# Optimization experiments

Measured on AMD Instinct MI355X. Metric: run time of the kernel, lower is better.

The kernel has to match this reference:

```python
import jax, jax.numpy as jnp
import numpy as np

# ---- static configuration (mirrors init_kwargs) ----
B, V, C, NH, HD = 1, 6, 256, 8, 32     # batch, views, embed, heads, head_dim
Z, L, P = 4, 4, 2                       # z-ref points, fmap levels, ref points
BEV_H, BEV_W = 80, 80
Q = BEV_H * BEV_W
IMG_H, IMG_W = 480, 800
LEVEL_SHAPES = [(60, 100), (30, 50), (15, 25), (8, 13)]
S = sum(h * w for h, w in LEVEL_SHAPES)
RES = 0.512
OFFSET_SCALE = 1.0
FF = 512


def layer_norm(x, g, b):
    m = jnp.mean(x, -1, keepdims=True)
    v = jnp.var(x, -1, keepdims=True)
    return (x - m) / jnp.sqrt(v + 1e-5) * g + b


def _bev_grid():
    xs = (jnp.arange(BEV_W) + 0.5) / BEV_W
    ys = (jnp.arange(BEV_H) + 0.5) / BEV_H
    gy, gx = jnp.meshgrid(ys, xs, indexing='ij')
    ref = jnp.stack([gx.reshape(-1), gy.reshape(-1)], -1)        # (Q,2) normalized xy
    world = (ref - 0.5) * jnp.array([BEV_W * RES, BEV_H * RES])  # (Q,2) ego-frame meters
    return ref, world


def deform_sample(value, H, W, loc):
    """Bilinear sampling. value: (N, H*W, NH, HD); loc: (N, Qn, NH, PP, 2) in [0,1].
    Returns (N, Qn, NH, PP, HD); out-of-bounds samples contribute zero."""
    v = jnp.moveaxis(value, 2, 1)                                # (N, NH, HW, HD)
    x = loc[..., 0] * W - 0.5
    y = loc[..., 1] * H - 0.5
    x0 = jnp.floor(x); y0 = jnp.floor(y)
    lx, ly = x - x0, y - y0
    x0 = x0.astype(jnp.int32); y0 = y0.astype(jnp.int32)
    gather = jax.vmap(jax.vmap(lambda vt, it: vt[it]))           # over (N, NH)
    def corner(xi, yi, w):
        ok = ((xi >= 0) & (xi < W) & (yi >= 0) & (yi < H)).astype(value.dtype)
        idx = jnp.clip(yi, 0, H - 1) * W + jnp.clip(xi, 0, W - 1)
        g = gather(v, jnp.moveaxis(idx, 2, 1))                   # (N,NH,Qn,PP,HD)
        return jnp.moveaxis(g, 1, 2) * (w * ok)[..., None]
    return (corner(x0, y0, (1 - lx) * (1 - ly)) + corner(x0 + 1, y0, lx * (1 - ly))
            + corner(x0, y0 + 1, (1 - lx) * ly) + corner(x0 + 1, y0 + 1, lx * ly))


def _forward(bev_queries, bev_histories, multiscale_fmaps, transition_matrices, z_refs,
             cam_proj_matrices, Wv_t, Woff_t, boff_t, Ww_t, bw_t, Wo_t, bo_t, ln1_g, ln1_b,
             Wv_s, Woff_s, boff_s, Ww_s, bw_s, Wo_s, bo_s, ln2_g, ln2_b,
             W1, b1, W2, b2, ln3_g, ln3_b):
    ref, world = _bev_grid()
    q = bev_queries
    # ---------- temporal self-attention (deformable over current + warped history) ----------
    vcur = (q @ Wv_t).reshape(B, Q, NH, HD)
    vhist = (bev_histories @ Wv_t).reshape(B, Q, NH, HD)
    off_t = (q @ Woff_t + boff_t).reshape(B, Q, NH, 2, P, 2) * OFFSET_SCALE
    w_t = jax.nn.softmax((q @ Ww_t + bw_t).reshape(B, Q, NH, 2 * P), -1).reshape(B, Q, NH, 2, P)
    ext = jnp.array([BEV_W * RES, BEV_H * RES], jnp.float32)
    wh = jnp.concatenate([world, jnp.ones((Q, 1), jnp.float32)], -1)     # (Q,3)
    warped = jnp.einsum('bij,qj->bqi', transition_matrices, wh)          # (B,Q,3)
    ref_hist = warped[..., :2] / warped[..., 2:3] / ext + 0.5            # (B,Q,2)
    norm_bev = jnp.array([BEV_W, BEV_H], jnp.float32)
    loc_c = ref[None, :, None, None, :] + off_t[:, :, :, 0] / norm_bev
    loc_h = ref_hist[:, :, None, None, :] + off_t[:, :, :, 1] / norm_bev
    s_c = deform_sample(vcur, BEV_H, BEV_W, loc_c)                       # (B,Q,NH,P,HD)
    s_h = deform_sample(vhist, BEV_H, BEV_W, loc_h)
    out_t = (jnp.einsum('bqhp,bqhpd->bqhd', w_t[:, :, :, 0], s_c)
             + jnp.einsum('bqhp,bqhpd->bqhd', w_t[:, :, :, 1], s_h))
    out1 = out_t.reshape(B, Q, C) @ Wo_t + bo_t
    out2 = layer_norm(out1 + q, ln1_g, ln1_b)
    # ---------- spatial cross-attention (multi-view multi-scale deformable) ----------
    val = (multiscale_fmaps @ Wv_s).reshape(B * V, S, NH, HD)
    pts = jnp.concatenate([
        jnp.broadcast_to(world[:, None, :], (Q, Z, 2)),
        jnp.broadcast_to(z_refs[None, :, None], (Q, Z, 1)),
        jnp.ones((Q, Z, 1), jnp.float32)], -1)                           # (Q,Z,4) homogeneous
    uvd = jnp.einsum('vij,qzj->vqzi', cam_proj_matrices, pts)            # (V,Q,Z,3)
    d = uvd[..., 2]
    un = uvd[..., 0] / jnp.maximum(d, 1e-5) / IMG_W
    vn = uvd[..., 1] / jnp.maximum(d, 1e-5) / IMG_H
    valid = ((d > 1e-5) & (un >= 0) & (un <= 1) & (vn >= 0) & (vn <= 1)).astype(q.dtype)
    refuv = jnp.stack([un, vn], -1)                                      # (V,Q,Z,2)
    off_s = (out2 @ Woff_s + boff_s).reshape(B, Q, NH, Z, L, P, 2) * OFFSET_SCALE
    w_s = jax.nn.softmax((out2 @ Ww_s + bw_s).reshape(B, Q, NH, Z * L * P), -1)
    w_s = w_s.reshape(B, Q, NH, Z, L, P)
    acc = jnp.zeros((B, Q, NH, HD), q.dtype)
    start = 0
    for l, (Hl, Wl) in enumerate(LEVEL_SHAPES):
        vl = val[:, start:start + Hl * Wl]
        start += Hl * Wl
        loc = (refuv[None, :, :, None, :, None, :]
               + off_s[:, None, :, :, :, l] / jnp.array([Wl, Hl], jnp.float32))
        loc = jnp.broadcast_to(loc, (B, V, Q, NH, Z, P, 2)).reshape(B * V, Q, NH, Z * P, 2)
        samp = deform_sample(vl, Hl, Wl, loc).reshape(B, V, Q, NH, Z, P, HD)
        wl = w_s[:, None, :, :, :, l] * valid[None, :, :, None, :, None]
        acc = acc + jnp.einsum('bvqhzp,bvqhzpd->bqhd', wl, samp)
    count = jnp.maximum(valid.sum((0, 2)), 1.0)                          # (Q,) hit count
    out3 = (acc / count[None, :, None, None]).reshape(B, Q, C) @ Wo_s + bo_s
    out4 = layer_norm(out3 + out2, ln2_g, ln2_b)
    # ---------- feed-forward ----------
    out5 = jax.nn.relu(out4 @ W1 + b1) @ W2 + b2
    return layer_norm(out5 + out4, ln3_g, ln3_b)


def setup_inputs() -> dict:
    key = jax.random.key(0)
    ks = iter(jax.random.split(key, 40))
    def rn(shape, s=1.0):
        return jax.random.normal(next(ks), shape, jnp.float32) * s
    sc = 1.0 / float(np.sqrt(C))
    inp = {}
    inp['bev_queries'] = rn((B, Q, C), 0.1)
    inp['bev_histories'] = rn((B, Q, C), 0.1)
    inp['multiscale_fmaps'] = rn((B, V, S, C), 0.1)
    th = 0.02
    T = np.array([[np.cos(th), -np.sin(th), 0.5],
                  [np.sin(th), np.cos(th), 0.1],
                  [0.0, 0.0, 1.0]], np.float32)
    inp['transition_matrices'] = jnp.tile(jnp.asarray(T)[None], (B, 1, 1))
    inp['z_refs'] = jnp.linspace(-5.0, 3.0, Z).astype(jnp.float32)
    K = np.array([[400.0, 0.0, IMG_W / 2], [0.0, 400.0, IMG_H / 2], [0.0, 0.0, 1.0]], np.float32)
    Ps = []
    for vi in range(V):
        a = 2 * np.pi * vi / V
        Rt = np.zeros((3, 4), np.float32)
        Rt[0, :3] = [-np.sin(a), np.cos(a), 0.0]   # camera right
        Rt[1, :3] = [0.0, 0.0, -1.0]               # camera down
        Rt[2, :3] = [np.cos(a), np.sin(a), 0.0]    # camera forward
        Ps.append(K @ Rt)
    inp['cam_proj_matrices'] = jnp.asarray(np.stack(Ps))
    # temporal self-attention params
    inp['Wv_t'] = rn((C, C), sc)
    inp['Woff_t'] = rn((C, NH * 2 * P * 2), sc * 0.1)
    inp['boff_t'] = jnp.zeros((NH * 2 * P * 2,), jnp.float32)
    inp['Ww_t'] = rn((C, NH * 2 * P), sc)
    inp['bw_t'] = jnp.zeros((NH * 2 * P,), jnp.float32)
    inp['Wo_t'] = rn((C, C), sc)
    inp['bo_t'] = jnp.zeros((C,), jnp.float32)
    inp['ln1_g'] = jnp.ones((C,), jnp.float32)
    inp['ln1_b'] = jnp.zeros((C,), jnp.float32)
    # spatial cross-attention params
    inp['Wv_s'] = rn((C, C), sc)
    inp['Woff_s'] = rn((C, NH * Z * L * P * 2), sc * 0.1)
    inp['boff_s'] = jnp.zeros((NH * Z * L * P * 2,), jnp.float32)
    inp['Ww_s'] = rn((C, NH * Z * L * P), sc)
    inp['bw_s'] = jnp.zeros((NH * Z * L * P,), jnp.float32)
    inp['Wo_s'] = rn((C, C), sc)
    inp['bo_s'] = jnp.zeros((C,), jnp.float32)
    inp['ln2_g'] = jnp.ones((C,), jnp.float32)
    inp['ln2_b'] = jnp.zeros((C,), jnp.float32)
    # FFN params
    inp['W1'] = rn((C, FF), sc)
    inp['b1'] = jnp.zeros((FF,), jnp.float32)
    inp['W2'] = rn((FF, C), 1.0 / float(np.sqrt(FF)))
    inp['b2'] = jnp.zeros((C,), jnp.float32)
    inp['ln3_g'] = jnp.ones((C,), jnp.float32)
    inp['ln3_b'] = jnp.zeros((C,), jnp.float32)
    # static shape descriptors (treated as compile-time constants)
    inp['bev_spatial_shape'] = np.array([[BEV_H, BEV_W]], np.int64)
    inp['multiscale_fmap_shapes'] = np.array(LEVEL_SHAPES, np.int64)
    inp['img_spatial_shape'] = np.array([[IMG_H, IMG_W]], np.int64)
    return inp


def reference(bev_queries, bev_histories, multiscale_fmaps, transition_matrices, z_refs,
              cam_proj_matrices, Wv_t, Woff_t, boff_t, Ww_t, bw_t, Wo_t, bo_t, ln1_g, ln1_b,
              Wv_s, Woff_s, boff_s, Ww_s, bw_s, Wo_s, bo_s, ln2_g, ln2_b,
              W1, b1, W2, b2, ln3_g, ln3_b,
              bev_spatial_shape, multiscale_fmap_shapes, img_spatial_shape):
    return _forward(bev_queries, bev_histories, multiscale_fmaps, transition_matrices, z_refs,
                    cam_proj_matrices, Wv_t, Woff_t, boff_t, Ww_t, bw_t, Wo_t, bo_t, ln1_g, ln1_b,
                    Wv_s, Woff_s, boff_s, Ww_s, bw_s, Wo_s, bo_s, ln2_g, ln2_b,
                    W1, b1, W2, b2, ln3_g, ln3_b)
```

## Files before the change

### kernel.cpp

```cpp
#include <hip/hip_runtime.h>
#include <hip/hip_bf16.h>
#include <hip/hip_fp16.h>

typedef unsigned short u16;
typedef unsigned int u32;
typedef __attribute__((ext_vector_type(8))) short bf16x8;
typedef __attribute__((ext_vector_type(4))) float f32x4;

#define Q_N  6400
#define S_N  7979
#define BEV  80

__device__ __forceinline__ float ubf(u16 u) {
    return __uint_as_float(((u32)u) << 16);
}
__device__ __forceinline__ u16 bfrn(float x) {
    u32 b = __float_as_uint(x);
    return (u16)((b + 0x7FFFu + ((b >> 16) & 1u)) >> 16);
}
__device__ __forceinline__ float f16tof(u16 u) {
    __half h; *(u16*)&h = u; return __half2float(h);
}
__device__ __forceinline__ u16 ftof16(float f) {
    __half h = __float2half(f); return *(u16*)&h;
}

template <int AIN, int RELU, int OUTMODE, int SM4, int SM32>
__device__ __forceinline__ void gemm_body(
    const void* __restrict__ A, const u16* __restrict__ WhT, const u16* __restrict__ WlT,
    const float* __restrict__ bias, const float* __restrict__ bias2,
    void* __restrict__ Cout, int M, int N, int K, int bx, int by,
    u16* Ah, u16* Al, u16* Wh, u16* Wl)
{
    const int tid  = threadIdx.x;
    const int lane = tid & 63;
    const int wave = tid >> 6;
    const int wm = (wave >> 1) * 32, wn = (wave & 1) * 64;
    const int m0 = by * 64, n0 = bx * 128;
    const int arow = tid >> 2, ak = (tid & 3) * 8;
    const int wrow = tid >> 1, wk = (tid & 1) * 16;
    const int fr = lane & 15, gq = lane >> 4;

    f32x4 acc[8];
    #pragma unroll
    for (int i = 0; i < 8; ++i) acc[i] = (f32x4)(0.f);

    for (int k0 = 0; k0 < K; k0 += 32) {
        {
// ... 29 lines not shown
        {
            const size_t wo = (size_t)(n0 + wrow) * K + k0 + wk;
            *(uint4*)&Wh[wrow * 40 + wk]     = *(const uint4*)(WhT + wo);
            *(uint4*)&Wh[wrow * 40 + wk + 8] = *(const uint4*)(WhT + wo + 8);
            *(uint4*)&Wl[wrow * 40 + wk]     = *(const uint4*)(WlT + wo);
            *(uint4*)&Wl[wrow * 40 + wk + 8] = *(const uint4*)(WlT + wo + 8);
        }
        __syncthreads();
        bf16x8 fah[2], fal[2], fwh[4], fwl[4];
        #pragma unroll
        for (int i = 0; i < 2; ++i) {
            fah[i] = *(const bf16x8*)&Ah[(wm + i * 16 + fr) * 40 + gq * 8];
            fal[i] = *(const bf16x8*)&Al[(wm + i * 16 + fr) * 40 + gq * 8];
        }
        #pragma unroll
        for (int j = 0; j < 4; ++j) {
            fwh[j] = *(const bf16x8*)&Wh[(wn + j * 16 + fr) * 40 + gq * 8];
            fwl[j] = *(const bf16x8*)&Wl[(wn + j * 16 + fr) * 40 + gq * 8];
        }
        #pragma unroll
        for (int i = 0; i < 2; ++i)
            #pragma unroll
            for (int j = 0; j < 4; ++j) {
                acc[i * 4 + j] = __builtin_amdgcn_mfma_f32_16x16x32_bf16(fah[i], fwh[j], acc[i * 4 + j], 0, 0, 0);
                acc[i * 4 + j] = __builtin_amdgcn_mfma_f32_16x16x32_bf16(fal[i], fwh[j], acc[i * 4 + j], 0, 0, 0);
                acc[i * 4 + j] = __builtin_amdgcn_mfma_f32_16x16x32_bf16(fah[i], fwl[j], acc[i * 4 + j], 0, 0, 0);
            }
        __syncthreads();
    }
    const int g4r = gq * 4;
    float bv[4];
    #pragma unroll
    for (int j = 0; j < 4; ++j) {
        int col = n0 + wn + j * 16 + fr;
        if (bias2) bv[j] = (col < 512) ? bias[col] : bias2[col - 512];
        else       bv[j] = bias ? bias[col] : 0.f;
    }
    const bool do_sm32 = SM32 && ((n0 + wn) >= 512);
    const bool do_sm4  = SM4 && (wn == 64);
    #pragma unroll
    for (int i = 0; i < 2; ++i) {
        #pragma unroll
        for (int r = 0; r < 4; ++r) {
            const int row = m0 + wm + i * 16 + g4r + r;
            float v0 = acc[i * 4 + 0][r] + bv[0];
            float v1 = acc[i * 4 + 1][r] + bv[1];
            float v2 = acc[i * 4 + 2][r] + bv[2];
            float v3 = acc[i * 4 + 3][r] + bv[3];
            if (RELU) {
                v0 = fmaxf(v0, 0.f); v1 = fmaxf(v1, 0.f);
                v2 = fmaxf(v2, 0.f); v3 = fmaxf(v3, 0.f);
            }
            if (SM4 && do_sm4) {
                float m0q = fmaxf(v0, __shfl_xor(v0, 1));
                m0q = fmaxf(m0q, __shfl_xor(m0q, 2));
                float e0 = __expf(v0 - m0q);
                float s0 = e0 + __shfl_xor(e0, 1);
                s0 += __shfl_xor(s0, 2);
                v0 = e0 / s0;
                float m1q = fmaxf(v1, __shfl_xor(v1, 1));
                m1q = fmaxf(m1q, __shfl_xor(m1q, 2));
                float e1 = __expf(v1 - m1q);
                float s1 = e1 + __shfl_xor(e1, 1);
                s1 += __shfl_xor(s1, 2);
                v1 = e1 / s1;
                v2 = 0.f; v3 = 0.f;
            }
            if (SM32 && do_sm32) {
                float ma = fmaxf(v0, v1);
                ma = fmaxf(ma, __shfl_xor(ma, 1));
                ma = fmaxf(ma, __shfl_xor(ma, 2));
                ma = fmaxf(ma, __shfl_xor(ma, 4));
                ma = fmaxf(ma, __shfl_xor(ma, 8));
                float e0 = __expf(v0 - ma), e1 = __expf(v1 - ma);
                float sa = e0 + e1;
                sa += __shfl_xor(sa, 1);
                sa += __shfl_xor(sa, 2);
                sa += __shfl_xor(sa, 4);
                sa += __shfl_xor(sa, 8);
                float ia = 1.f / sa;
                v0 = e0 * ia; v1 = e1 * ia;
                float mb = fmaxf(v2, v3);
                mb = fmaxf(mb, __shfl_xor(mb, 1));
                mb = fmaxf(mb, __shfl_xor(mb, 2));
                mb = fmaxf(mb, __shfl_xor(mb, 4));
                mb = fmaxf(mb, __shfl_xor(mb, 8));
                float e2 = __expf(v2 - mb), e3 = __expf(v3 - mb);
                float sb = e2 + e3;
                sb += __shfl_xor(sb, 1);
                sb += __shfl_xor(sb, 2);
                sb += __shfl_xor(sb, 4);
                sb += __shfl_xor(sb, 8);
                float ib = 1.f / sb;
                v2 = e2 * ib; v3 = e3 * ib;
            }
            if (row < M) {
                const int colb = n0 + wn + fr;
                if (OUTMODE == 1) {
                    u16* cp = (u16*)Cout + (size_t)row * N;
                    cp[colb]      = ftof16(v0);
                    cp[colb + 16] = ftof16(v1);
                    cp[colb + 32] = ftof16(v2);
                    cp[colb + 48] = ftof16(v3);
                } else {
                    float* cp = (float*)Cout + (size_t)row * N;
                    cp[colb]      = v0;
                    cp[colb + 16] = v1;
                    cp[colb + 32] = v2;
                    cp[colb + 48] = v3;
                }
            }
        }
    }
}

template <int AIN, int OUTMODE>
__device__ __forceinline__ void gemm_body256(
    const void* __restrict__ A, const u16* __restrict__ WhT, const u16* __restrict__ WlT,
    const float* __restrict__ bias, void* __restrict__ Cout, int M, int K, int by, u16* smem)
{
    u16* Ah = smem;
    u16* Al = smem + 2560;
    u16* Wh = smem + 5120;
    u16* Wl = smem + 15360;
    const int tid  = threadIdx.x;
    const int lane = tid & 63;
    const int wave = tid >> 6;
    const int wm = (wave >> 1) * 32, wn = (wave & 1) * 128;
    const int m0 = by * 64;
    const int arow = tid >> 2, ak = (tid & 3) * 8;
    const int fr = lane & 15, gq = lane >> 4;

    f32x4 acc[16];
    #pragma unroll
    for (int i = 0; i < 16; ++i) acc[i] = (f32x4)(0.f);

    for (int k0 = 0; k0 < K; k0 += 32) {
        {
            const bool okr = (m0 + arow) < M;
            float vals[8];
            if (AIN == 0) {
                const float* ap = (const float*)A + (size_t)(m0 + arow) * K + k0 + ak;
                float4 v0 = okr ? *(const float4*)(ap)     : make_float4(0.f, 0.f, 0.f, 0.f);
                float4 v1 = okr ? *(const float4*)(ap + 4) : make_float4(0.f, 0.f, 0.f, 0.f);
                vals[0] = v0.x; vals[1] = v0.y; vals[2] = v0.z; vals[3] = v0.w;
                vals[4] = v1.x; vals[5] = v1.y; vals[6] = v1.z; vals[7] = v1.w;
            } else {
                const u16* ap = (const u16*)A + (size_t)(m0 + arow) * K + k0 + ak;
                uint4 u = okr ? *(const uint4*)ap : make_uint4(0, 0, 0, 0);
                const __half2* hp = (const __half2*)&u;
                #pragma unroll
                for (int i = 0; i < 4; ++i) {
                    float2 f = __half22float2(hp[i]);
                    vals[2 * i] = f.x; vals[2 * i + 1] = f.y;
                }
            }
            u16 hb[8], lb[8];
            #pragma unroll
            for (int i = 0; i < 8; ++i) {
                hb[i] = bfrn(vals[i]);
                lb[i] = bfrn(vals[i] - ubf(hb[i]));
            }
            *(ushort4*)(&Ah[arow * 40 + ak])     = *(ushort4*)&hb[0];
            *(ushort4*)(&Ah[arow * 40 + ak + 4]) = *(ushort4*)&hb[4];
            *(ushort4*)(&Al[arow * 40 + ak])     = *(ushort4*)&lb[0];
            *(ushort4*)(&Al[arow * 40 + ak + 4]) = *(ushort4*)&lb[4];
        }
        {
            const size_t wo = (size_t)tid * K + k0;
            const uint4* sh = (const uint4*)(WhT + wo);
            const uint4* sl = (const uint4*)(WlT + wo);
            uint4* dh = (uint4*)&Wh[tid * 40];
            uint4* dl = (uint4*)&Wl[tid * 40];
            dh[0] = sh[0]; dh[1] = sh[1]; dh[2] = sh[2]; dh[3] = sh[3];
            dl[0] = sl[0]; dl[1] = sl[1]; dl[2] = sl[2]; dl[3] = sl[3];
        }
        __syncthreads();
        bf16x8 fah[2], fal[2];
        #pragma unroll
        for (int i = 0; i < 2; ++i) {
            fah[i] = *(const bf16x8*)&Ah[(wm + i * 16 + fr) * 40 + gq * 8];
            fal[i] = *(const bf16x8*)&Al[(wm + i * 16 + fr) * 40 + gq * 8];
        }
        #pragma unroll
        for (int jg = 0; jg < 2; ++jg) {
            bf16x8 fwh[4], fwl[4];
            #pragma unroll
            for (int j = 0; j < 4; ++j) {
                fwh[j] = *(const bf16x8*)&Wh[(wn + jg * 64 + j * 16 + fr) * 40 + gq * 8];
                fwl[j] = *(const bf16x8*)&Wl[(wn + jg * 64 + j * 16 + fr) * 40 + gq * 8];
            }
            #pragma unroll
            for (int i = 0; i < 2; ++i)
                #pragma unroll
                for (int j = 0; j < 4; ++j) {
                    int a = i * 8 + jg * 4 + j;
                    acc[a] = __builtin_amdgcn_mfma_f32_16x16x32_bf16(fah[i], fwh[j], acc[a], 0, 0, 0);
                    acc[a] = __builtin_amdgcn_mfma_f32_16x16x32_bf16(fal[i], fwh[j], acc[a], 0, 0, 0);
                    acc[a] = __builtin_amdgcn_mfma_f32_16x16x32_bf16(fah[i], fwl[j], acc[a], 0, 0, 0);
                }
        }
        __syncthreads();
    }
    const int g4r = gq * 4;
    #pragma unroll
    for (int i = 0; i < 2; ++i) {
        #pragma unroll
        for (int r = 0; r < 4; ++r) {
            const int row = m0 + wm + i * 16 + g4r + r;
            if (row >= M) continue;
            #pragma unroll
            for (int j = 0; j < 8; ++j) {
                int col = wn + j * 16 + fr;
                float v = acc[i * 8 + j][r] + (bias ? bias[col] : 0.f);
                if (OUTMODE == 1) ((u16*)Cout)[(size_t)row * 256 + col] = ftof16(v);
                else              ((float*)Cout)[(size_t)row * 256 + col] = v;
            }
        }
    }
}

template <int AIN, int RELU, int OUTMODE, int SM32>
__global__ __launch_bounds__(256) void mgemm_k(
    const void* __restrict__ A, const u16* __restrict__ WhT, const u16* __restrict__ WlT,
    const float* __restrict__ bias, const float* __restrict__ bias2,
    void* __restrict__ Cout, int M, int N, int K)
{
    __shared__ u16 smem[15360];
    gemm_body<AIN, RELU, OUTMODE, 0, SM32>(A, WhT, WlT, bias, bias2, Cout,
                                           M, N, K, blockIdx.x, blockIdx.y,
                                           smem, smem + 2560, smem + 5120, smem + 10240);
}

__global__ __launch_bounds__(256) void fused3_k(
    const float* __restrict__ fmaps, const float* __restrict__ q, const float* __restrict__ hist,
    const u16* __restrict__ Wv_s_h, const u16* __restrict__ Wv_s_l,
    const u16* __restrict__ Wv_t_h, const u16* __restrict__ Wv_t_l,
    const u16* __restrict__ Wc_h,   const u16* __restrict__ Wc_l,
    const float* __restrict__ bc,
    u16* __restrict__ val_f16, u16* __restrict__ vcur, u16* __restrict__ vhist,
    float* __restrict__ owt)
{
    __shared__ u16 smem[25600];
    const int b = blockIdx.x;
    if (b < 749) {
        gemm_body256<0, 1>(fmaps, Wv_s_h, Wv_s_l, nullptr, val_f16, 47874, 256, b, smem);
    } else if (b < 849) {
        gemm_body256<0, 1>(q, Wv_t_h, Wv_t_l, nullptr, vcur, 6400, 256, b - 749, smem);
    } else if (b < 949) {
        gemm_body256<0, 1>(hist, Wv_t_h, Wv_t_l, nullptr, vhist, 6400, 256, b - 849, smem);
    } else {
        gemm_body<0, 0, 0, 1, 0>(q, Wc_h, Wc_l, bc, nullptr, owt,
                                 6400, 128, 256, 0, b - 949,
                                 smem, smem + 2560, smem + 5120, smem + 10240);
    }
}

__global__ __launch_bounds__(256) void wprep_k(
    const float* __restrict__ w0, const float* __restrict__ w1, const float* __restrict__ w2,
    const float* __restrict__ w3, const float* __restrict__ w4, const float* __restrict__ w5,
    const float* __restrict__ w6, const float* __restrict__ w7, u16* __restrict__ base,
    const float* __restrict__ Woff_t, const float* __restrict__ Ww_t,
    const float* __restrict__ boff_t, const float* __restrict__ bw_t,
    float* __restrict__ bc)
{
    const int b = blockIdx.x, tid = threadIdx.x;
    if (b == 184) {
        if (tid < 128) bc[tid] = (tid < 64) ? boff_t[tid] : (tid < 96 ? bw_t[tid - 64] : 0.f);
        return;
    }
    const int cum[10]  = {0, 16, 32, 48, 80, 96, 112, 144, 176, 184};
    const int Ks[9]    = {256, 256, 256, 256, 256, 256, 256, 512, 256};
    const int Ns[9]    = {256, 256, 256, 512, 256, 256, 512, 256, 128};
    const int hoff[9]  = {0, 131072, 262144, 393216, 524288, 786432, 917504, 1179648, 1441792};
    const int loff[9]  = {65536, 196608, 327680, 589824, 720896, 851968, 1048576, 1310720, 1474560};
    int seg = 0;
    #pragma unroll
// ... 22 lines not shown
            float v = (n < 64) ? Woff_t[k * 64 + n] : (n < 96 ? Ww_t[k * 32 + n - 64] : 0.f);
            tile[rr][cc + i] = v;
        }
    }
    __syncthreads();
    const int nr = tid >> 2, kc = (tid & 3) * 16;
    u16 hb[16], lb[16];
    #pragma unroll
    for (int i = 0; i < 16; ++i) {
        float v = tile[kc + i][nr];
        hb[i] = bfrn(v);
        lb[i] = bfrn(v - ubf(hb[i]));
    }
    u16* hp = base + hoff[seg] + (size_t)(n0 + nr) * K + k0 + kc;
    u16* lp = base + loff[seg] + (size_t)(n0 + nr) * K + k0 + kc;
    *(ushort4*)(hp + 0)  = *(ushort4*)&hb[0];
    *(ushort4*)(hp + 4)  = *(ushort4*)&hb[4];
    *(ushort4*)(hp + 8)  = *(ushort4*)&hb[8];
    *(ushort4*)(hp + 12) = *(ushort4*)&hb[12];
    *(ushort4*)(lp + 0)  = *(ushort4*)&lb[0];
    *(ushort4*)(lp + 4)  = *(ushort4*)&lb[4];
    *(ushort4*)(lp + 8)  = *(ushort4*)&lb[8];
    *(ushort4*)(lp + 12) = *(ushort4*)&lb[12];
}

__global__ __launch_bounds__(256) void ln_k(
    const float* __restrict__ x, const float* __restrict__ res,
    const float* __restrict__ g, const float* __restrict__ b,
    float* __restrict__ out)
{
    const int row = blockIdx.x, t = threadIdx.x;
    const size_t idx = (size_t)row * 256 + t;
    float v = x[idx] + res[idx];
    float s = v, ss = v * v;
    #pragma unroll
    for (int o = 32; o > 0; o >>= 1) {
        s += __shfl_down(s, o);
        ss += __shfl_down(ss, o);
    }
    __shared__ float red[8];
    __shared__ float mv[2];
    const int wv = t >> 6, ln = t & 63;
    if (ln == 0) { red[wv] = s; red[4 + wv] = ss; }
    __syncthreads();
    if (t == 0) {
        float S = red[0] + red[1] + red[2] + red[3];
        float SS = red[4] + red[5] + red[6] + red[7];
        float mean = S * (1.f / 256.f);
        float var = SS * (1.f / 256.f) - mean * mean;
        mv[0] = mean;
        mv[1] = rsqrtf(var + 1e-5f);
    }
    __syncthreads();
    out[idx] = (v - mv[0]) * mv[1] * g[t] + b[t];
}

__device__ __forceinline__ float4 bilin4h(const u16* __restrict__ v, int H, int W,
                                          float x, float y, int chb)
{
    float xf = floorf(x), yf = floorf(y);
    int x0 = (int)xf, y0 = (int)yf;
    int x1 = x0 + 1, y1 = y0 + 1;
    float fx = x - xf, fy = y - yf;
    float w00 = (1.f - fx) * (1.f - fy), w10 = fx * (1.f - fy);
    float w01 = (1.f - fx) * fy,         w11 = fx * fy;
    bool xi0 = (x0 >= 0) && (x0 < W);
    bool xi1 = (x1 >= 0) && (x1 < W);
    bool yi0 = (y0 >= 0) && (y0 < H);
    bool yi1 = (y1 >= 0) && (y1 < H);
    float4 r = make_float4(0.f, 0.f, 0.f, 0.f);
    #define CORNER(xi, yi, xx, yy, ww)                                           \
        if ((yi) && (xi)) {                                                      \
            uint2 u = *(const uint2*)(v + ((size_t)(yy) * W + (xx)) * 256 + chb);\
            float2 f0 = __half22float2(*(const __half2*)&u.x);                   \
            float2 f1 = __half22float2(*(const __half2*)&u.y);                   \
            r.x += (ww) * f0.x; r.y += (ww) * f0.y;                              \
            r.z += (ww) * f1.x; r.w += (ww) * f1.y;                              \
// ... 187 lines not shown
    const float* fmaps  = (const float*)d_in[2];
    const float* Tm     = (const float*)d_in[3];
    const float* zrefs  = (const float*)d_in[4];
    const float* cam    = (const float*)d_in[5];
    const float* Woff_t = (const float*)d_in[7];
    const float* boff_t = (const float*)d_in[8];
    const float* Ww_t   = (const float*)d_in[9];
    const float* bw_t   = (const float*)d_in[10];
    const float* bo_t   = (const float*)d_in[12];
    const float* ln1g   = (const float*)d_in[13];
    const float* ln1b   = (const float*)d_in[14];
    const float* boff_s = (const float*)d_in[17];
    const float* bw_s   = (const float*)d_in[19];
    const float* bo_s   = (const float*)d_in[21];
    const float* ln2g   = (const float*)d_in[22];
    const float* ln2b   = (const float*)d_in[23];
    const float* b1     = (const float*)d_in[25];
    const float* b2     = (const float*)d_in[27];
    const float* ln3g   = (const float*)d_in[28];
    const float* ln3b   = (const float*)d_in[29];

    float* ws    = (float*)d_ws;
    float* r0    = ws;
    float* r1    = ws + 1638400;
    float* owt   = ws + 3276800;
    float* r4    = ws + 4096000;
    u16*  r5u    = (u16*)(ws + 5734400);
    float* of4   = ws + 8192000;
    u16*  valbuf = (u16*)(ws + 9830400);
    u16*  vcur   = (u16*)(ws + 15958272);
    u16*  vhist  = (u16*)(ws + 16777472);
    u16*  wtab   = (u16*)(ws + 17596672);
    float* bc    = ws + 18350336;

    u16* hidden = valbuf;
    u16* Wv_t_h = wtab + 0,       *Wv_t_l = wtab + 65536;
    u16* Wo_t_h = wtab + 131072,  *Wo_t_l = wtab + 196608;
    u16* Wv_s_h = wtab + 262144,  *Wv_s_l = wtab + 327680;
    u16* Comb_h = wtab + 393216,  *Comb_l = wtab + 589824;
    u16* Wo_s_h = wtab + 786432,  *Wo_s_l = wtab + 851968;
    u16* W1_h   = wtab + 917504,  *W1_l   = wtab + 1048576;
    u16* W2_h   = wtab + 1179648, *W2_l   = wtab + 1310720;
    u16* Wc_h   = wtab + 1441792, *Wc_l   = wtab + 1474560;

    dim3 blk(256);
    auto gm = [](int M, int N) { return dim3((unsigned)(N / 128), (unsigned)((M + 63) / 64)); };

    wprep_k<<<dim3(185), blk, 0, stream>>>(
        (const float*)d_in[6], (const float*)d_in[11], (const float*)d_in[15],
        (const float*)d_in[16], (const float*)d_in[18], (const float*)d_in[20],
        (const float*)d_in[24], (const float*)d_in[26], wtab,
        Woff_t, Ww_t, boff_t, bw_t, bc);
    fused3_k<<<dim3(1049), blk, 0, stream>>>(
        fmaps, q, hist, Wv_s_h, Wv_s_l, Wv_t_h, Wv_t_l, Wc_h, Wc_l, bc,
        valbuf, vcur, vhist, owt);
    temporal_k<<<dim3(6400), blk, 0, stream>>>(vcur, vhist, owt, Tm, r4);
    mgemm_k<0,0,0,0><<<gm(6400, 256), blk, 0, stream>>>(
        r4, Wo_t_h, Wo_t_l, bo_t, nullptr, r0, 6400, 256, 256);
    ln_k<<<dim3(6400), blk, 0, stream>>>(r0, q, ln1g, ln1b, r1);
    mgemm_k<0,0,1,1><<<gm(6400, 768), blk, 0, stream>>>(
        r1, Comb_h, Comb_l, boff_s, bw_s, r5u, 6400, 768, 256);
    spatial_k<<<dim3(6400), blk, 0, stream>>>(valbuf, r5u, cam, zrefs, r0);
    mgemm_k<0,0,0,0><<<gm(6400, 256), blk, 0, stream>>>(
        r0, Wo_s_h, Wo_s_l, bo_s, nullptr, r4, 6400, 256, 256);
    ln_k<<<dim3(6400), blk, 0, stream>>>(r4, r1, ln2g, ln2b, of4);
    mgemm_k<0,1,1,0><<<gm(6400, 512), blk, 0, stream>>>(
        of4, W1_h, W1_l, b1, nullptr, hidden, 6400, 512, 256);
    mgemm_k<1,0,0,0><<<gm(6400, 256), blk, 0, stream>>>(
        hidden, W2_h, W2_l, b2, nullptr, r0, 6400, 256, 512);
    ln_k<<<dim3(6400), blk, 0, stream>>>(r0, of4, ln3g, ln3b, (float*)d_out);
}
```

Measured before the change: 360.5 us.

## Fuse post-attention GEMM, LayerNorm and FFN chains into two row-block megakernels

Replaces the separate output-projection GEMMs, LayerNorm kernels and FFN GEMMs with two kernels (megaA, megaB). Each handles 16 rows end to end, keeping the normalized rows and the FFN hidden activations in shared memory as fp16. This removes several launches and the global round-trips of intermediate activations. The value-projection GEMMs in fused3 also move from 64x256 tiles to 64x128 tiles, doubling the block count. In exchange, only 400 blocks run the fused stages, and every block restages the full weight matrices from global memory. Storing the residual and hidden rows as fp16 in LDS may also cost some precision.

```diff
diff --git a/kernel.cpp b/kernel.cpp
--- a/kernel.cpp
+++ b/kernel.cpp
@@ -24,6 +24,11 @@
 __device__ __forceinline__ u16 ftof16(float f) {
     __half h = __float2half(f); return *(u16*)&h;
 }
+
+#define MFMA3(a, fa_h, fa_l, fw_h, fw_l)                                          \
+    a = __builtin_amdgcn_mfma_f32_16x16x32_bf16(fa_h, fw_h, a, 0, 0, 0);          \
+    a = __builtin_amdgcn_mfma_f32_16x16x32_bf16(fa_l, fw_h, a, 0, 0, 0);          \
+    a = __builtin_amdgcn_mfma_f32_16x16x32_bf16(fa_h, fw_l, a, 0, 0, 0);
 
 template <int AIN, int RELU, int OUTMODE, int SM4, int SM32>
 __device__ __forceinline__ void gemm_body(
@@ -99,9 +104,7 @@
         for (int i = 0; i < 2; ++i)
             #pragma unroll
             for (int j = 0; j < 4; ++j) {
-                acc[i * 4 + j] = __builtin_amdgcn_mfma_f32_16x16x32_bf16(fah[i], fwh[j], acc[i * 4 + j], 0, 0, 0);
-                acc[i * 4 + j] = __builtin_amdgcn_mfma_f32_16x16x32_bf16(fal[i], fwh[j], acc[i * 4 + j], 0, 0, 0);
-                acc[i * 4 + j] = __builtin_amdgcn_mfma_f32_16x16x32_bf16(fah[i], fwl[j], acc[i * 4 + j], 0, 0, 0);
+                MFMA3(acc[i * 4 + j], fah[i], fal[i], fwh[j], fwl[j]);
             }
         __syncthreads();
     }
@@ -110,11 +113,9 @@
     #pragma unroll
     for (int j = 0; j < 4; ++j) {
         int col = n0 + wn + j * 16 + fr;
-        if (bias2) bv[j] = (col < 512) ? bias[col] : bias2[col - 512];
-        else       bv[j] = bias ? bias[col] : 0.f;
-    }
-    const bool do_sm32 = SM32 && ((n0 + wn) >= 512);
-    const bool do_sm4  = SM4 && (wn == 64);
+        bv[j] = bias ? bias[col] : 0.f;
+    }
+    const bool do_sm4 = SM4 && (wn == 64);
     #pragma unroll
     for (int i = 0; i < 2; ++i) {
         #pragma unroll
@@ -143,7 +144,197 @@
                 v1 = e1 / s1;
                 v2 = 0.f; v3 = 0.f;
             }
-            if (SM32 && do_sm32) {
+            if (row < M) {
+                const int colb = n0 + wn + fr;
+                if (OUTMODE == 1) {
+                    u16* cp = (u16*)Cout + (size_t)row * N;
+                    cp[colb]      = ftof16(v0);
+                    cp[colb + 16] = ftof16(v1);
+                    cp[colb + 32] = ftof16(v2);
+                    cp[colb + 48] = ftof16(v3);
+                } else {
+                    float* cp = (float*)Cout + (size_t)row * N;
+                    cp[colb]      = v0;
+                    cp[colb + 16] = v1;
+                    cp[colb + 32] = v2;
+                    cp[colb + 48] = v3;
+                }
+            }
+        }
+    }
+}
+
+__global__ __launch_bounds__(256) void fused3_k(
+    const float* __restrict__ fmaps, const float* __restrict__ q, const float* __restrict__ hist,
+    const u16* __restrict__ Wv_s_h, const u16* __restrict__ Wv_s_l,
+    const u16* __restrict__ Wv_t_h, const u16* __restrict__ Wv_t_l,
+    const u16* __restrict__ Wc_h,   const u16* __restrict__ Wc_l,
+    const float* __restrict__ bc,
+    u16* __restrict__ val_f16, u16* __restrict__ vcur, u16* __restrict__ vhist,
+    float* __restrict__ owt)
+{
+    __shared__ u16 smem[15360];
+    const int b = blockIdx.x;
+    if (b < 1498) {
+        gemm_body<0, 0, 1, 0, 0>(fmaps, Wv_s_h, Wv_s_l, nullptr, nullptr, val_f16,
+                                 47874, 256, 256, b & 1, b >> 1,
+                                 smem, smem + 2560, smem + 5120, smem + 10240);
+    } else if (b < 1698) {
+        int l = b - 1498;
+        gemm_body<0, 0, 1, 0, 0>(q, Wv_t_h, Wv_t_l, nullptr, nullptr, vcur,
+                                 6400, 256, 256, l & 1, l >> 1,
+                                 smem, smem + 2560, smem + 5120, smem + 10240);
+    } else if (b < 1898) {
+        int l = b - 1698;
+        gemm_body<0, 0, 1, 0, 0>(hist, Wv_t_h, Wv_t_l, nullptr, nullptr, vhist,
+                                 6400, 256, 256, l & 1, l >> 1,
+                                 smem, smem + 2560, smem + 5120, smem + 10240);
+    } else {
+        int l = b - 1898;
+        gemm_body<0, 0, 0, 1, 0>(q, Wc_h, Wc_l, bc, nullptr, owt,
+                                 6400, 128, 256, 0, l,
+                                 smem, smem + 2560, smem + 5120, smem + 10240);
+    }
+}
+
+__device__ __forceinline__ void stageW256(const u16* __restrict__ WhT, const u16* __restrict__ WlT,
+                                          int nbase, int K, int k0, u16* Wh, u16* Wl)
+{
+    const int t = threadIdx.x;
+    const size_t wo = (size_t)(nbase + t) * K + k0;
+    const uint4* sh = (const uint4*)(WhT + wo);
+    const uint4* sl = (const uint4*)(WlT + wo);
+    uint4* dh = (uint4*)&Wh[t * 40];
+    uint4* dl = (uint4*)&Wl[t * 40];
+    dh[0] = sh[0]; dh[1] = sh[1]; dh[2] = sh[2]; dh[3] = sh[3];
+    dl[0] = sl[0]; dl[1] = sl[1]; dl[2] = sl[2]; dl[3] = sl[3];
+}
+
+__device__ __forceinline__ void stageA16(const float* __restrict__ A, int m0, int K, int k0,
+                                         u16* Ah, u16* Al)
+{
+    const int t = threadIdx.x;
+    if (t < 128) {
+        const int row = t >> 3, kq = (t & 7) * 4;
+        float4 v = *(const float4*)(A + (size_t)(m0 + row) * K + k0 + kq);
+        ushort4 h, l;
+        h.x = bfrn(v.x); l.x = bfrn(v.x - ubf(h.x));
+        h.y = bfrn(v.y); l.y = bfrn(v.y - ubf(h.y));
+        h.z = bfrn(v.z); l.z = bfrn(v.z - ubf(h.z));
+        h.w = bfrn(v.w); l.w = bfrn(v.w - ubf(h.w));
+        *(ushort4*)&Ah[row * 40 + kq] = h;
+        *(ushort4*)&Al[row * 40 + kq] = l;
+    }
+}
+
+__device__ __forceinline__ void splitf16x8(const u16* __restrict__ src, bf16x8& hi, bf16x8& lo)
+{
+    uint4 u = *(const uint4*)src;
+    const __half2* hp = (const __half2*)&u;
+    u16 hb[8], lb[8];
+    #pragma unroll
+    for (int i = 0; i < 4; ++i) {
+        float2 f = __half22float2(hp[i]);
+        hb[2 * i]     = bfrn(f.x); lb[2 * i]     = bfrn(f.x - ubf(hb[2 * i]));
+        hb[2 * i + 1] = bfrn(f.y); lb[2 * i + 1] = bfrn(f.y - ubf(hb[2 * i + 1]));
+    }
+    hi = *(bf16x8*)hb; lo = *(bf16x8*)lb;
+}
+
+__global__ __launch_bounds__(256) void megaA_k(
+    const float* __restrict__ outt, const float* __restrict__ q,
+    const u16* __restrict__ Wo_t_h, const u16* __restrict__ Wo_t_l, const float* __restrict__ bo_t,
+    const float* __restrict__ ln1g, const float* __restrict__ ln1b,
+    const u16* __restrict__ Comb_h, const u16* __restrict__ Comb_l,
+    const float* __restrict__ boff_s, const float* __restrict__ bw_s,
+    float* __restrict__ out2, u16* __restrict__ r5u)
+{
+    __shared__ u16 Wh[256 * 40], Wl[256 * 40];
+    __shared__ u16 Ah[16 * 40], Al[16 * 40];
+    __shared__ u16 stash[16 * 264];
+    __shared__ float sredS[64], sredQ[64];
+    const int tid = threadIdx.x, lane = tid & 63, wave = tid >> 6;
+    const int fr = lane & 15, gq = lane >> 4;
+    const int wn = wave * 64;
+    const int m0 = blockIdx.x * 16;
+
+    f32x4 acc[4];
+    #pragma unroll
+    for (int j = 0; j < 4; ++j) acc[j] = (f32x4)(0.f);
+    for (int k0 = 0; k0 < 256; k0 += 32) {
+        stageA16(outt, m0, 256, k0, Ah, Al);
+        stageW256(Wo_t_h, Wo_t_l, 0, 256, k0, Wh, Wl);
+        __syncthreads();
+        bf16x8 fah = *(const bf16x8*)&Ah[fr * 40 + gq * 8];
+        bf16x8 fal = *(const bf16x8*)&Al[fr * 40 + gq * 8];
+        #pragma unroll
+        for (int j = 0; j < 4; ++j) {
+            bf16x8 fwh = *(const bf16x8*)&Wh[(wn + j * 16 + fr) * 40 + gq * 8];
+            bf16x8 fwl = *(const bf16x8*)&Wl[(wn + j * 16 + fr) * 40 + gq * 8];
+            MFMA3(acc[j], fah, fal, fwh, fwl);
+        }
+        __syncthreads();
+    }
+    #pragma unroll
+    for (int r = 0; r < 4; ++r) {
+        const int rl = gq * 4 + r, row = m0 + rl;
+        float s = 0.f, ss = 0.f;
+        #pragma unroll
+        for (int j = 0; j < 4; ++j) {
+            const int col = wn + j * 16 + fr;
+            float v = acc[j][r] + bo_t[col] + q[(size_t)row * 256 + col];
+            acc[j][r] = v;
+            s += v; ss += v * v;
+        }
+        s += __shfl_xor(s, 1); ss += __shfl_xor(ss, 1);
+        s += __shfl_xor(s, 2); ss += __shfl_xor(ss, 2);
+        s += __shfl_xor(s, 4); ss += __shfl_xor(ss, 4);
+        s += __shfl_xor(s, 8); ss += __shfl_xor(ss, 8);
+        if (fr == 0) { sredS[rl * 4 + wave] = s; sredQ[rl * 4 + wave] = ss; }
+    }
+    __syncthreads();
+    #pragma unroll
+    for (int r = 0; r < 4; ++r) {
+        const int rl = gq * 4 + r, row = m0 + rl;
+        float S  = sredS[rl * 4] + sredS[rl * 4 + 1] + sredS[rl * 4 + 2] + sredS[rl * 4 + 3];
+        float SS = sredQ[rl * 4] + sredQ[rl * 4 + 1] + sredQ[rl * 4 + 2] + sredQ[rl * 4 + 3];
+        float mean = S * (1.f / 256.f);
+        float rstd = rsqrtf(SS * (1.f / 256.f) - mean * mean + 1e-5f);
+        #pragma unroll
+        for (int j = 0; j < 4; ++j) {
+            const int col = wn + j * 16 + fr;
+            float o = (acc[j][r] - mean) * rstd * ln1g[col] + ln1b[col];
+            out2[(size_t)row * 256 + col] = o;
+            stash[rl * 264 + col] = ftof16(o);
+        }
+    }
+    __syncthreads();
+    for (int pass = 0; pass < 3; ++pass) {
+        f32x4 a2[4];
+        #pragma unroll
+        for (int j = 0; j < 4; ++j) a2[j] = (f32x4)(0.f);
+        for (int k0 = 0; k0 < 256; k0 += 32) {
+            stageW256(Comb_h, Comb_l, pass * 256, 256, k0, Wh, Wl);
+            __syncthreads();
+            bf16x8 fah, fal;
+            splitf16x8(&stash[fr * 264 + k0 + gq * 8], fah, fal);
+            #pragma unroll
+            for (int j = 0; j < 4; ++j) {
+                bf16x8 fwh = *(const bf16x8*)&Wh[(wn + j * 16 + fr) * 40 + gq * 8];
+                bf16x8 fwl = *(const bf16x8*)&Wl[(wn + j * 16 + fr) * 40 + gq * 8];
+                MFMA3(a2[j], fah, fal, fwh, fwl);
+            }
+            __syncthreads();
+        }
+        #pragma unroll
+        for (int r = 0; r < 4; ++r) {
+            const int rl = gq * 4 + r, row = m0 + rl;
+            const int c0 = pass * 256 + wn + fr;
+            float v0 = a2[0][r] + ((c0      < 512) ? boff_s[c0]      : bw_s[c0 - 512]);
+            float v1 = a2[1][r] + ((c0 + 16 < 512) ? boff_s[c0 + 16] : bw_s[c0 + 16 - 512]);
+            float v2 = a2[2][r] + ((c0 + 32 < 512) ? boff_s[c0 + 32] : bw_s[c0 + 32 - 512]);
+            float v3 = a2[3][r] + ((c0 + 48 < 512) ? boff_s[c0 + 48] : bw_s[c0 + 48 - 512]);
+            if (pass == 2) {
                 float ma = fmaxf(v0, v1);
                 ma = fmaxf(ma, __shfl_xor(ma, 1));
                 ma = fmaxf(ma, __shfl_xor(ma, 2));
@@ -171,165 +362,156 @@
                 float ib = 1.f / sb;
                 v2 = e2 * ib; v3 = e3 * ib;
             }
-            if (row < M) {
-                const int colb = n0 + wn + fr;
-                if (OUTMODE == 1) {
-                    u16* cp = (u16*)Cout + (size_t)row * N;
-                    cp[colb]      = ftof16(v0);
-                    cp[colb + 16] = ftof16(v1);
-                    cp[colb + 32] = ftof16(v2);
-                    cp[colb + 48] = ftof16(v3);
-                } else {
-                    float* cp = (float*)Cout + (size_t)row * N;
-                    cp[colb]      = v0;
-                    cp[colb + 16] = v1;
-                    cp[colb + 32] = v2;
-                    cp[colb + 48] = v3;
-                }
-            }
-        }
-    }
-}
-
-template <int AIN, int OUTMODE>
-__device__ __forceinline__ void gemm_body256(
-    const void* __restrict__ A, const u16* __restrict__ WhT, const u16* __restrict__ WlT,
-    const float* __restrict__ bias, void* __restrict__ Cout, int M, int K, int by, u16* smem)
-{
-    u16* Ah = smem;
-    u16* Al = smem + 2560;
-    u16* Wh = smem + 5120;
-    u16* Wl = smem + 15360;
-    const int tid  = threadIdx.x;
-    const int lane = tid & 63;
-    const int wave = tid >> 6;
-    const int wm = (wave >> 1) * 32, wn = (wave & 1) * 128;
-    const int m0 = by * 64;
-    const int arow = tid >> 2, ak = (tid & 3) * 8;
+            u16* rp = r5u + (size_t)row * 768 + pass * 256 + wn + fr;
+            rp[0]  = ftof16(v0); rp[16] = ftof16(v1);
+            rp[32] = ftof16(v2); rp[48] = ftof16(v3);
+        }
+    }
+}
+
+__global__ __launch_bounds__(256) void megaB_k(
+    const float* __restrict__ samp, const float* __restrict__ out2,
+    const u16* __restrict__ Wo_s_h, const u16* __restrict__ Wo_s_l, const float* __restrict__ bo_s,
+    const float* __restrict__ ln2g, const float* __restrict__ ln2b,
+    const u16* __restrict__ W1_h, const u16* __restrict__ W1_l, const float* __restrict__ b1,
+    const u16* __restrict__ W2_h, const u16* __restrict__ W2_l, const float* __restrict__ b2,
+    const float* __restrict__ ln3g, const float* __restrict__ ln3b,
+    float* __restrict__ dout)
+{
+    __shared__ u16 Wh[256 * 40], Wl[256 * 40];
+    __shared__ u16 Ah[16 * 40], Al[16 * 40];
+    __shared__ u16 stash[16 * 264];
+    __shared__ u16 hidden[16 * 520];
+    __shared__ float sredS[64], sredQ[64];
+    const int tid = threadIdx.x, lane = tid & 63, wave = tid >> 6;
     const int fr = lane & 15, gq = lane >> 4;
-
-    f32x4 acc[16];
-    #pragma unroll
-    for (int i = 0; i < 16; ++i) acc[i] = (f32x4)(0.f);
-
-    for (int k0 = 0; k0 < K; k0 += 32) {
-        {
-            const bool okr = (m0 + arow) < M;
-            float vals[8];
-            if (AIN == 0) {
-                const float* ap = (const float*)A + (size_t)(m0 + arow) * K + k0 + ak;
-                float4 v0 = okr ? *(const float4*)(ap)     : make_float4(0.f, 0.f, 0.f, 0.f);
-                float4 v1 = okr ? *(const float4*)(ap + 4) : make_float4(0.f, 0.f, 0.f, 0.f);
-                vals[0] = v0.x; vals[1] = v0.y; vals[2] = v0.z; vals[3] = v0.w;
-                vals[4] = v1.x; vals[5] = v1.y; vals[6] = v1.z; vals[7] = v1.w;
-            } else {
-                const u16* ap = (const u16*)A + (size_t)(m0 + arow) * K + k0 + ak;
-                uint4 u = okr ? *(const uint4*)ap : make_uint4(0, 0, 0, 0);
-                const __half2* hp = (const __half2*)&u;
-                #pragma unroll
-                for (int i = 0; i < 4; ++i) {
-                    float2 f = __half22float2(hp[i]);
-                    vals[2 * i] = f.x; vals[2 * i + 1] = f.y;
-                }
-            }
-            u16 hb[8], lb[8];
-            #pragma unroll
-            for (int i = 0; i < 8; ++i) {
-                hb[i] = bfrn(vals[i]);
-                lb[i] = bfrn(vals[i] - ubf(hb[i]));
-            }
-            *(ushort4*)(&Ah[arow * 40 + ak])     = *(ushort4*)&hb[0];
-            *(ushort4*)(&Ah[arow * 40 + ak + 4]) = *(ushort4*)&hb[4];
-            *(ushort4*)(&Al[arow * 40 + ak])     = *(ushort4*)&lb[0];
-            *(ushort4*)(&Al[arow * 40 + ak + 4]) = *(ushort4*)&lb[4];
-        }
-        {
-            const size_t wo = (size_t)tid * K + k0;
-            const uint4* sh = (const uint4*)(WhT + wo);
-            const uint4* sl = (const uint4*)(WlT + wo);
-            uint4* dh = (uint4*)&Wh[tid * 40];
-            uint4* dl = (uint4*)&Wl[tid * 40];
-            dh[0] = sh[0]; dh[1] = sh[1]; dh[2] = sh[2]; dh[3] = sh[3];
-            dl[0] = sl[0]; dl[1] = sl[1]; dl[2] = sl[2]; dl[3] = sl[3];
-        }
+    const int wn = wave * 64;
+    const int m0 = blockIdx.x * 16;
+
+    f32x4 acc[4];
+    #pragma unroll
+    for (int j = 0; j < 4; ++j) acc[j] = (f32x4)(0.f);
+    for (int k0 = 0; k0 < 256; k0 += 32) {
+        stageA16(samp, m0, 256, k0, Ah, Al);
+        stageW256(Wo_s_h, Wo_s_l, 0, 256, k0, Wh, Wl);
         __syncthreads();
-        bf16x8 fah[2], fal[2];
-        #pragma unroll
-        for (int i = 0; i < 2; ++i) {
-            fah[i] = *(const bf16x8*)&Ah[(wm + i * 16 + fr) * 40 + gq * 8];
-            fal[i] = *(const bf16x8*)&Al[(wm + i * 16 + fr) * 40 + gq * 8];
-        }
-        #pragma unroll
-        for (int jg = 0; jg < 2; ++jg) {
-            bf16x8 fwh[4], fwl[4];
+        bf16x8 fah = *(const bf16x8*)&Ah[fr * 40 + gq * 8];
+        bf16x8 fal = *(const bf16x8*)&Al[fr * 40 + gq * 8];
+        #pragma unroll
+        for (int j = 0; j < 4; ++j) {
+            bf16x8 fwh = *(const bf16x8*)&Wh[(wn + j * 16 + fr) * 40 + gq * 8];
+            bf16x8 fwl = *(const bf16x8*)&Wl[(wn + j * 16 + fr) * 40 + gq * 8];
+            MFMA3(acc[j], fah, fal, fwh, fwl);
+        }
+        __syncthreads();
+    }
+    #pragma unroll
+    for (int r = 0; r < 4; ++r) {
+        const int rl = gq * 4 + r, row = m0 + rl;
+        float s = 0.f, ss = 0.f;
+        #pragma unroll
+        for (int j = 0; j < 4; ++j) {
+            const int col = wn + j * 16 + fr;
+            float v = acc[j][r] + bo_s[col] + out2[(size_t)row * 256 + col];
+            acc[j][r] = v;
+            s += v; ss += v * v;
+        }
+        s += __shfl_xor(s, 1); ss += __shfl_xor(ss, 1);
+        s += __shfl_xor(s, 2); ss += __shfl_xor(ss, 2);
+        s += __shfl_xor(s, 4); ss += __shfl_xor(ss, 4);
+        s += __shfl_xor(s, 8); ss += __shfl_xor(ss, 8);
+        if (fr == 0) { sredS[rl * 4 + wave] = s; sredQ[rl * 4 + wave] = ss; }
+    }
+    __syncthreads();
+    #pragma unroll
+    for (int r = 0; r < 4; ++r) {
+        const int rl = gq * 4 + r;
+        float S  = sredS[rl * 4] + sredS[rl * 4 + 1] + sredS[rl * 4 + 2] + sredS[rl * 4 + 3];
+        float SS = sredQ[rl * 4] + sredQ[rl * 4 + 1] + sredQ[rl * 4 + 2] + sredQ[rl * 4 + 3];
+        float mean = S * (1.f / 256.f);
+        float rstd = rsqrtf(SS * (1.f / 256.f) - mean * mean + 1e-5f);
+        #pragma unroll
+        for (int j = 0; j < 4; ++j) {
+            const int col = wn + j * 16 + fr;
+            float o = (acc[j][r] - mean) * rstd * ln2g[col] + ln2b[col];
+            stash[rl * 264 + col] = ftof16(o);
+        }
+    }
+    __syncthreads();
+    for (int pass = 0; pass < 2; ++pass) {
+        f32x4 a2[4];
+        #pragma unroll
+        for (int j = 0; j < 4; ++j) a2[j] = (f32x4)(0.f);
+        for (int k0 = 0; k0 < 256; k0 += 32) {
+            stageW256(W1_h, W1_l, pass * 256, 256, k0, Wh, Wl);
+            __syncthreads();
+            bf16x8 fah, fal;
+            splitf16x8(&stash[fr * 264 + k0 + gq * 8], fah, fal);
             #pragma unroll
             for (int j = 0; j < 4; ++j) {
-                fwh[j] = *(const bf16x8*)&Wh[(wn + jg * 64 + j * 16 + fr) * 40 + gq * 8];
-                fwl[j] = *(const bf16x8*)&Wl[(wn + jg * 64 + j * 16 + fr) * 40 + gq * 8];
-            }
+                bf16x8 fwh = *(const bf16x8*)&Wh[(wn + j * 16 + fr) * 40 + gq * 8];
+                bf16x8 fwl = *(const bf16x8*)&Wl[(wn + j * 16 + fr) * 40 + gq * 8];
+                MFMA3(a2[j], fah, fal, fwh, fwl);
+            }
+            __syncthreads();
+        }
+        #pragma unroll
+        for (int r = 0; r < 4; ++r) {
+            const int rl = gq * 4 + r;
             #pragma unroll
-            for (int i = 0; i < 2; ++i)
-                #pragma unroll
-                for (int j = 0; j < 4; ++j) {
-                    int a = i * 8 + jg * 4 + j;
-                    acc[a] = __builtin_amdgcn_mfma_f32_16x16x32_bf16(fah[i], fwh[j], acc[a], 0, 0, 0);
-                    acc[a] = __builtin_amdgcn_mfma_f32_16x16x32_bf16(fal[i], fwh[j], acc[a], 0, 0, 0);
-                    acc[a] = __builtin_amdgcn_mfma_f32_16x16x32_bf16(fah[i], fwl[j], acc[a], 0, 0, 0);
-                }
-        }
+            for (int j = 0; j < 4; ++j) {
+                const int col = pass * 256 + wn + j * 16 + fr;
+                float v = fmaxf(a2[j][r] + b1[col], 0.f);
+                hidden[rl * 520 + col] = ftof16(v);
+            }
+        }
+    }
+    __syncthreads();
+    #pragma unroll
+    for (int j = 0; j < 4; ++j) acc[j] = (f32x4)(0.f);
+    for (int k0 = 0; k0 < 512; k0 += 32) {
+        stageW256(W2_h, W2_l, 0, 512, k0, Wh, Wl);
         __syncthreads();
-    }
-    const int g4r = gq * 4;
-    #pragma unroll
-    for (int i = 0; i < 2; ++i) {
-        #pragma unroll
-        for (int r = 0; r < 4; ++r) {
-            const int row = m0 + wm + i * 16 + g4r + r;
-            if (row >= M) continue;
-            #pragma unroll
-            for (int j = 0; j < 8; ++j) {
-                int col = wn + j * 16 + fr;
-                float v = acc[i * 8 + j][r] + (bias ? bias[col] : 0.f);
-                if (OUTMODE == 1) ((u16*)Cout)[(size_t)row * 256 + col] = ftof16(v);
-                else              ((float*)Cout)[(size_t)row * 256 + col] = v;
-            }
-        }
-    }
-}
-
-template <int AIN, int RELU, int OUTMODE, int SM32>
-__global__ __launch_bounds__(256) void mgemm_k(
-    const void* __restrict__ A, const u16* __restrict__ WhT, const u16* __restrict__ WlT,
-    const float* __restrict__ bias, const float* __restrict__ bias2,
-    void* __restrict__ Cout, int M, int N, int K)
-{
-    __shared__ u16 smem[15360];
-    gemm_body<AIN, RELU, OUTMODE, 0, SM32>(A, WhT, WlT, bias, bias2, Cout,
-                                           M, N, K, blockIdx.x, blockIdx.y,
-                                           smem, smem + 2560, smem + 5120, smem + 10240);
-}
-
-__global__ __launch_bounds__(256) void fused3_k(
-    const float* __restrict__ fmaps, const float* __restrict__ q, const float* __restrict__ hist,
-    const u16* __restrict__ Wv_s_h, const u16* __restrict__ Wv_s_l,
-    const u16* __restrict__ Wv_t_h, const u16* __restrict__ Wv_t_l,
-    const u16* __restrict__ Wc_h,   const u16* __restrict__ Wc_l,
-    const float* __restrict__ bc,
-    u16* __restrict__ val_f16, u16* __restrict__ vcur, u16* __restrict__ vhist,
-    float* __restrict__ owt)
-{
-    __shared__ u16 smem[25600];
-    const int b = blockIdx.x;
-    if (b < 749) {
-        gemm_body256<0, 1>(fmaps, Wv_s_h, Wv_s_l, nullptr, val_f16, 47874, 256, b, smem);
-    } else if (b < 849) {
-        gemm_body256<0, 1>(q, Wv_t_h, Wv_t_l, nullptr, vcur, 6400, 256, b - 749, smem);
-    } else if (b < 949) {
-        gemm_body256<0, 1>(hist, Wv_t_h, Wv_t_l, nullptr, vhist, 6400, 256, b - 849, smem);
-    } else {
-        gemm_body<0, 0, 0, 1, 0>(q, Wc_h, Wc_l, bc, nullptr, owt,
-                                 6400, 128, 256, 0, b - 949,
-                                 smem, smem + 2560, smem + 5120, smem + 10240);
+        bf16x8 fah, fal;
+        splitf16x8(&hidden[fr * 520 + k0 + gq * 8], fah, fal);
+        #pragma unroll
+        for (int j = 0; j < 4; ++j) {
+            bf16x8 fwh = *(const bf16x8*)&Wh[(wn + j * 16 + fr) * 40 + gq * 8];
+            bf16x8 fwl = *(const bf16x8*)&Wl[(wn + j * 16 + fr) * 40 + gq * 8];
+            MFMA3(acc[j], fah, fal, fwh, fwl);
+        }
+        __syncthreads();
+    }
+    #pragma unroll
+    for (int r = 0; r < 4; ++r) {
+        const int rl = gq * 4 + r;
+        float s = 0.f, ss = 0.f;
+        #pragma unroll
+        for (int j = 0; j < 4; ++j) {
+            const int col = wn + j * 16 + fr;
+            float v = acc[j][r] + b2[col] + f16tof(stash[rl * 264 + col]);
+            acc[j][r] = v;
+            s += v; ss += v * v;
+        }
+        s += __shfl_xor(s, 1); ss += __shfl_xor(ss, 1);
+        s += __shfl_xor(s, 2); ss += __shfl_xor(ss, 2);
+        s += __shfl_xor(s, 4); ss += __shfl_xor(ss, 4);
+        s += __shfl_xor(s, 8); ss += __shfl_xor(ss, 8);
+        if (fr == 0) { sredS[rl * 4 + wave] = s; sredQ[rl * 4 + wave] = ss; }
+    }
+    __syncthreads();
+    #pragma unroll
+    for (int r = 0; r < 4; ++r) {
+        const int rl = gq * 4 + r, row = m0 + rl;
+        float S  = sredS[rl * 4] + sredS[rl * 4 + 1] + sredS[rl * 4 + 2] + sredS[rl * 4 + 3];
+        float SS = sredQ[rl * 4] + sredQ[rl * 4 + 1] + sredQ[rl * 4 + 2] + sredQ[rl * 4 + 3];
+        float mean = S * (1.f / 256.f);
+        float rstd = rsqrtf(SS * (1.f / 256.f) - mean * mean + 1e-5f);
+        #pragma unroll
+        for (int j = 0; j < 4; ++j) {
+            const int col = wn + j * 16 + fr;
+            dout[(size_t)row * 256 + col] = (acc[j][r] - mean) * rstd * ln3g[col] + ln3b[col];
+        }
     }
 }
 
@@ -398,37 +580,6 @@
     *(ushort4*)(lp + 4)  = *(ushort4*)&lb[4];
     *(ushort4*)(lp + 8)  = *(ushort4*)&lb[8];
     *(ushort4*)(lp + 12) = *(ushort4*)&lb[12];
-}
-
-__global__ __launch_bounds__(256) void ln_k(
-    const float* __restrict__ x, const float* __restrict__ res,
-    const float* __restrict__ g, const float* __restrict__ b,
-    float* __restrict__ out)
-{
-    const int row = blockIdx.x, t = threadIdx.x;
-    const size_t idx = (size_t)row * 256 + t;
-    float v = x[idx] + res[idx];
-    float s = v, ss = v * v;
-    #pragma unroll
-    for (int o = 32; o > 0; o >>= 1) {
-        s += __shfl_down(s, o);
-        ss += __shfl_down(ss, o);
-    }
-    __shared__ float red[8];
-    __shared__ float mv[2];
-    const int wv = t >> 6, ln = t & 63;
-    if (ln == 0) { red[wv] = s; red[4 + wv] = ss; }
-    __syncthreads();
-    if (t == 0) {
-        float S = red[0] + red[1] + red[2] + red[3];
-        float SS = red[4] + red[5] + red[6] + red[7];
-        float mean = S * (1.f / 256.f);
-        float var = SS * (1.f / 256.f) - mean * mean;
-        mv[0] = mean;
-        mv[1] = rsqrtf(var + 1e-5f);
-    }
-    __syncthreads();
-    out[idx] = (v - mv[0]) * mv[1] * g[t] + b[t];
 }
 
 __device__ __forceinline__ float4 bilin4h(const u16* __restrict__ v, int H, int W,
@@ -662,18 +813,16 @@
 
     float* ws    = (float*)d_ws;
     float* r0    = ws;
-    float* r1    = ws + 1638400;
+    float* out2  = ws + 1638400;
     float* owt   = ws + 3276800;
     float* r4    = ws + 4096000;
     u16*  r5u    = (u16*)(ws + 5734400);
-    float* of4   = ws + 8192000;
     u16*  valbuf = (u16*)(ws + 9830400);
     u16*  vcur   = (u16*)(ws + 15958272);
     u16*  vhist  = (u16*)(ws + 16777472);
     u16*  wtab   = (u16*)(ws + 17596672);
     float* bc    = ws + 18350336;
 
-    u16* hidden = valbuf;
     u16* Wv_t_h = wtab + 0,       *Wv_t_l = wtab + 65536;
     u16* Wo_t_h = wtab + 131072,  *Wo_t_l = wtab + 196608;
     u16* Wv_s_h = wtab + 262144,  *Wv_s_l = wtab + 327680;
@@ -684,29 +833,21 @@
     u16* Wc_h   = wtab + 1441792, *Wc_l   = wtab + 1474560;
 
     dim3 blk(256);
-    auto gm = [](int M, int N) { return dim3((unsigned)(N / 128), (unsigned)((M + 63) / 64)); };
 
     wprep_k<<<dim3(185), blk, 0, stream>>>(
         (const float*)d_in[6], (const float*)d_in[11], (const float*)d_in[15],
         (const float*)d_in[16], (const float*)d_in[18], (const float*)d_in[20],
         (const float*)d_in[24], (const float*)d_in[26], wtab,
         Woff_t, Ww_t, boff_t, bw_t, bc);
-    fused3_k<<<dim3(1049), blk, 0, stream>>>(
+    fused3_k<<<dim3(1998), blk, 0, stream>>>(
         fmaps, q, hist, Wv_s_h, Wv_s_l, Wv_t_h, Wv_t_l, Wc_h, Wc_l, bc,
         valbuf, vcur, vhist, owt);
     temporal_k<<<dim3(6400), blk, 0, stream>>>(vcur, vhist, owt, Tm, r4);
-    mgemm_k<0,0,0,0><<<gm(6400, 256), blk, 0, stream>>>(
-        r4, Wo_t_h, Wo_t_l, bo_t, nullptr, r0, 6400, 256, 256);
-    ln_k<<<dim3(6400), blk, 0, stream>>>(r0, q, ln1g, ln1b, r1);
-    mgemm_k<0,0,1,1><<<gm(6400, 768), blk, 0, stream>>>(
-        r1, Comb_h, Comb_l, boff_s, bw_s, r5u, 6400, 768, 256);
+    megaA_k<<<dim3(400), blk, 0, stream>>>(
+        r4, q, Wo_t_h, Wo_t_l, bo_t, ln1g, ln1b,
+        Comb_h, Comb_l, boff_s, bw_s, out2, r5u);
     spatial_k<<<dim3(6400), blk, 0, stream>>>(valbuf, r5u, cam, zrefs, r0);
-    mgemm_k<0,0,0,0><<<gm(6400, 256), blk, 0, stream>>>(
-        r0, Wo_s_h, Wo_s_l, bo_s, nullptr, r4, 6400, 256, 256);
-    ln_k<<<dim3(6400), blk, 0, stream>>>(r4, r1, ln2g, ln2b, of4);
-    mgemm_k<0,1,1,0><<<gm(6400, 512), blk, 0, stream>>>(
-        of4, W1_h, W1_l, b1, nullptr, hidden, 6400, 512, 256);
-    mgemm_k<1,0,0,0><<<gm(6400, 256), blk, 0, stream>>>(
-        hidden, W2_h, W2_l, b2, nullptr, r0, 6400, 256, 512);
-    ln_k<<<dim3(6400), blk, 0, stream>>>(r0, of4, ln3g, ln3b, (float*)d_out);
-}
+    megaB_k<<<dim3(400), blk, 0, stream>>>(
+        r0, out2, Wo_s_h, Wo_s_l, bo_s, ln2g, ln2b,
+        W1_h, W1_l, b1, W2_h, W2_l, b2, ln3g, ln3b, (float*)d_out);
+}
```

Result: slower. 396.8 us (+10.1%).
